# Performance work log

Measured on AMD Instinct MI355X. Metric: run time of the kernel, lower is better.

The kernel has to match this reference:

```python
import jax, jax.numpy as jnp
import numpy as np

S, B, W, D2 = 128, 64, 32, 512   # sen_len, batch, wiki_len, 2*eh_size
DH = 512                          # dh_size


def setup_inputs() -> dict:
    key = jax.random.key(0)
    ks = jax.random.split(key, 8)
    inp = {
        "i": 0,
        "valid_sen": jnp.arange(B, dtype=jnp.int64) if jax.config.jax_enable_x64 else jnp.arange(B, dtype=jnp.int32),
        "reverse_valid_sen": jnp.arange(B, dtype=jnp.int32),
        "wiki_sen": jax.random.randint(ks[0], (B, W, S), 0, 32000),
        "wiki_num": jax.random.randint(ks[1], (B,), 0, W),
        "h1": jax.random.normal(ks[2], (S, B, W, D2), dtype=jnp.float32),
        "h_n1": jax.random.normal(ks[3], (W, B, D2), dtype=jnp.float32),
        "atten_label": jax.random.randint(ks[4], (B,), 0, W),
        "h": jax.random.normal(ks[5], (B, D2), dtype=jnp.float32),
        "h_n": jax.random.normal(ks[6], (B, D2), dtype=jnp.float32),
        # initLinearLayer: Linear(4*eh -> dh)
        "W_init": jax.random.normal(ks[7], (DH, 2 * D2), dtype=jnp.float32) / np.sqrt(2 * D2),
        "b_init": jnp.zeros((DH,), dtype=jnp.float32),
    }
    inp["valid_sen"] = jnp.arange(B, dtype=jnp.int32)
    return inp


def reference(i, valid_sen, reverse_valid_sen, wiki_sen, wiki_num, h1, h_n1,
              atten_label, h, h_n, W_init, b_init):
    # --- gather valid sentences (index_select) ---
    vw_hn1 = h_n1[:, valid_sen]        # [W, Bv, D2]
    v_wiki_sen = wiki_sen[valid_sen]   # [Bv, W, S]
    v_h1 = h1[:, valid_sen]            # [S, Bv, W, D2]
    lbl = atten_label[valid_sen]       # [Bv]

    # --- attention scores: beta[b, w] = <h_n1[w, b], h_n[b]> ---
    beta = jnp.einsum('wbd,bd->bw', vw_hn1, h_n)  # [Bv, W]

    # --- CrossEntropyLoss(ignore_index=0) ---
    logp = jax.nn.log_softmax(beta, axis=1)
    nll = -jnp.take_along_axis(logp, lbl[:, None], axis=1)[:, 0]   # [Bv]
    valid = (lbl != 0)
    cnt = valid.sum().astype(beta.dtype)
    atten_loss = jnp.where(cnt > 0,
                           jnp.sum(jnp.where(valid, nll, 0.0)) / jnp.maximum(cnt, 1.0),
                           0.0)

    # --- golden (scatter one-hot) hard alignment -> context vector ---
    Bv = beta.shape[0]
    b_idx = jnp.arange(Bv)
    wiki_cv = vw_hn1[lbl, b_idx]                   # [Bv, D2]  (== sum over one-hot)

    # --- init hidden for decoder ---
    init_h = jnp.concatenate([h_n, wiki_cv], axis=1) @ W_init.T + b_init  # [Bv, DH]

    # --- select aligned wiki sentence / hidden states ---
    selected_wiki_h = v_h1[:, b_idx, lbl].transpose(1, 0, 2)  # [Bv, S, D2]
    selected_wiki_sen = v_wiki_sen[b_idx, lbl]                # [Bv, S]

    return (selected_wiki_sen, selected_wiki_h, init_h, wiki_cv, atten_loss)
```

## Files before the change

### kernel.cpp

```cpp
#include <hip/hip_runtime.h>

#define S 128
#define B 64
#define W 32
#define D2 512
#define DH 512

typedef float floatx4 __attribute__((ext_vector_type(4)));

#define OFF_SEN 0
#define OFF_SWH (B * S)
#define OFF_INITH (OFF_SWH + B * S * D2)
#define OFF_CV (OFF_INITH + B * DH)
#define OFF_LOSS (OFF_CV + B * D2)


#define NB_BETA 64
#define NB_INITH 128
#define NB_GATHER 512
#define NB_TOTAL (NB_BETA + NB_INITH + NB_GATHER)

__global__ __launch_bounds__(256) void k_fused(
    const float* __restrict__ h1, const float* __restrict__ h_n1,
    const float* __restrict__ h_n, const float* __restrict__ Wi,
    const float* __restrict__ bi, const int* __restrict__ wiki_sen,
    const int* __restrict__ valid_sen, const int* __restrict__ atten_label,
    float* __restrict__ out, float* __restrict__ ws)
{
    __shared__ float smem[4 * 2 * D2];
    const int bid = blockIdx.x;
    const int tid = threadIdx.x;

    if (bid < NB_BETA) {
        const int b = bid;
        const int lane = tid & 63;
        const int wv = tid >> 6;
        const int vs = valid_sen[b];
        const int lbl = atten_label[vs];
        float* sbeta = smem;

        const float* hb = h_n + b * D2;
        const float4 hn0 = ((const float4*)hb)[lane];
        const float4 hn1 = ((const float4*)hb)[64 + lane];

        #pragma unroll
        for (int i = 0; i < 8; ++i) {
            const int w = wv * 8 + i;
            const float* row = h_n1 + (w * B + vs) * D2;
            const float4 a0 = ((const float4*)row)[lane];
            const float4 a1 = ((const float4*)row)[64 + lane];
            float p = a0.x * hn0.x + a0.y * hn0.y + a0.z * hn0.z + a0.w * hn0.w
                    + a1.x * hn1.x + a1.y * hn1.y + a1.z * hn1.z + a1.w * hn1.w;
            #pragma unroll
            for (int m = 32; m >= 1; m >>= 1) p += __shfl_xor(p, m);
            if (lane == 0) sbeta[w] = p;
        }

        if (tid < 128) {
            const float4* src = (const float4*)(h_n1 + (lbl * B + vs) * D2);
            float4* dst = (float4*)(out + OFF_CV + b * D2);
            dst[tid] = src[tid];
        } else {
            const int s = tid - 128;
            out[OFF_SEN + b * S + s] = (float)wiki_sen[(vs * W + lbl) * S + s];
        }
        __syncthreads();

        if (tid == 0) {
            float mx = sbeta[0];
            for (int w = 1; w < W; ++w) mx = fmaxf(mx, sbeta[w]);
            float Z = 0.0f;
            for (int w = 0; w < W; ++w) Z += expf(sbeta[w] - mx);
            const float nll = -(sbeta[lbl] - mx - logf(Z));
            ws[b] = nll;
            ws[B + b] = (lbl != 0) ? 1.0f : 0.0f;
        }
    } else if (bid < NB_BETA + NB_INITH) {
        float (*wrow)[2 * D2] = (float (*)[2 * D2])smem;
        const int kt = (bid - NB_BETA) * 4;

        #pragma unroll
        for (int kk = 0; kk < 4; ++kk) {
            ((float4*)wrow[kk])[tid] =
                ((const float4*)(Wi + (size_t)(kt + kk) * (2 * D2)))[tid];
        }
        __syncthreads();

        const int b = tid >> 2;
        const int kk = tid & 3;
        const int k = kt + kk;
        const int vs = valid_sen[b];
        const int lbl = atten_label[vs];
        float acc = bi[k];
        const float4* hb = (const float4*)(h_n + b * D2);
        const float4* cb = (const float4*)(h_n1 + (lbl * B + vs) * D2);
        const float4* w0 = (const float4*)wrow[kk];
        const float4* w1 = (const float4*)(wrow[kk] + D2);
        #pragma unroll 4
        for (int d = 0; d < D2 / 4; ++d) {
            const float4 a = hb[d], w = w0[d];
            acc += a.x * w.x + a.y * w.y + a.z * w.z + a.w * w.w;
        }
        #pragma unroll 4
        for (int d = 0; d < D2 / 4; ++d) {
            const float4 a = cb[d], w = w1[d];
            acc += a.x * w.x + a.y * w.y + a.z * w.z + a.w * w.w;
        }
        out[OFF_INITH + b * DH + k] = acc;
    } else {
        const int gb = bid - NB_BETA - NB_INITH;
        const int b = gb >> 3;
        const int vs = valid_sen[b];
        const int gi = vs * W + atten_label[vs];

        floatx4 v[8];
        int q[8];
        #pragma unroll
        for (int j = 0; j < 8; ++j) {
            q[j] = gb * 2048 + j * 256 + tid;
            const int t = q[j] >> 7;
            const int s = t & 127;
            const int d4 = q[j] & 127;
            const floatx4* src =
                (const floatx4*)(h1 + ((size_t)(s * (B * W) + gi)) * D2);
            v[j] = __builtin_nontemporal_load(&src[d4]);
        }
        #pragma unroll
        for (int j = 0; j < 8; ++j) {
            __builtin_nontemporal_store(v[j], &((floatx4*)(out + OFF_SWH))[q[j]]);
        }
    }
}

__global__ void k_loss(const float* __restrict__ ws, float* __restrict__ out)
{
    const int t = threadIdx.x;
    float nll = ws[t];
    float v = ws[B + t];
    float sn = v * nll;
    float sc = v;
    #pragma unroll
    for (int m = 32; m >= 1; m >>= 1) {
        sn += __shfl_xor(sn, m);
        sc += __shfl_xor(sc, m);
    }
    if (t == 0) out[OFF_LOSS] = (sc > 0.0f) ? sn / fmaxf(sc, 1.0f) : 0.0f;
}

extern "C" void kernel_launch(void* const* d_in, const int* in_sizes, int n_in,
                              void* d_out, int out_size, void* d_ws, size_t ws_size,
                              hipStream_t stream) {
    const int* valid_sen   = (const int*)d_in[1];
    const int* wiki_sen    = (const int*)d_in[3];
    const float* h1        = (const float*)d_in[5];
    const float* h_n1      = (const float*)d_in[6];
    const int* atten_label = (const int*)d_in[7];
    const float* h_n       = (const float*)d_in[9];
    const float* Wi        = (const float*)d_in[10];
    const float* bi        = (const float*)d_in[11];
    float* out = (float*)d_out;
    float* ws  = (float*)d_ws;

    k_fused<<<NB_TOTAL, 256, 0, stream>>>(h1, h_n1, h_n, Wi, bi, wiki_sen,
                                          valid_sen, atten_label, out, ws);
    k_loss<<<1, 64, 0, stream>>>(ws, out);
}
```

Baseline: 22.00 us.

## Spread the h1 gather across all blocks with a grid-stride split

Every block (beta, init_h, and plain) now takes part in the big selected_wiki_h gather. It uses a grid-stride index with up to 6 float4 loads per thread instead of 8 per thread in dedicated blocks. This balances memory traffic across all 704 blocks so the beta and init_h blocks also contribute bandwidth. In exchange, those blocks carry more work and a longer tail, and each iteration now does per-element index lookups of valid_sen and atten_label.

```diff
diff --git a/kernel.cpp b/kernel.cpp
--- a/kernel.cpp
+++ b/kernel.cpp
@@ -17,8 +17,12 @@
 
 #define NB_BETA 64
 #define NB_INITH 128
-#define NB_GATHER 512
-#define NB_TOTAL (NB_BETA + NB_INITH + NB_GATHER)
+#define NB_PLAIN 512
+#define NB_TOTAL (NB_BETA + NB_INITH + NB_PLAIN)
+
+#define Q_TOTAL (B * S * (D2 / 4))
+#define GSTRIDE (NB_TOTAL * 256)
+#define GCHUNK 6
 
 __global__ __launch_bounds__(256) void k_fused(
     const float* __restrict__ h1, const float* __restrict__ h_n1,
@@ -107,27 +111,32 @@
             acc += a.x * w.x + a.y * w.y + a.z * w.z + a.w * w.w;
         }
         out[OFF_INITH + b * DH + k] = acc;
-    } else {
-        const int gb = bid - NB_BETA - NB_INITH;
-        const int b = gb >> 3;
-        const int vs = valid_sen[b];
-        const int gi = vs * W + atten_label[vs];
+    }
 
-        floatx4 v[8];
-        int q[8];
+    {
+        const int g0 = bid * 256 + tid;
+        floatx4 v[GCHUNK];
+        int q[GCHUNK];
+        bool ok[GCHUNK];
         #pragma unroll
-        for (int j = 0; j < 8; ++j) {
-            q[j] = gb * 2048 + j * 256 + tid;
-            const int t = q[j] >> 7;
-            const int s = t & 127;
-            const int d4 = q[j] & 127;
-            const floatx4* src =
-                (const floatx4*)(h1 + ((size_t)(s * (B * W) + gi)) * D2);
-            v[j] = __builtin_nontemporal_load(&src[d4]);
+        for (int j = 0; j < GCHUNK; ++j) {
+            q[j] = g0 + j * GSTRIDE;
+            ok[j] = (q[j] < Q_TOTAL);
+            if (ok[j]) {
+                const int t = q[j] >> 7;
+                const int s = t & 127;
+                const int b = t >> 7;
+                const int vs = valid_sen[b];
+                const int gi = vs * W + atten_label[vs];
+                const floatx4* src =
+                    (const floatx4*)(h1 + ((size_t)(s * (B * W) + gi)) * D2);
+                v[j] = __builtin_nontemporal_load(&src[q[j] & 127]);
+            }
         }
         #pragma unroll
-        for (int j = 0; j < 8; ++j) {
-            __builtin_nontemporal_store(v[j], &((floatx4*)(out + OFF_SWH))[q[j]]);
+        for (int j = 0; j < GCHUNK; ++j) {
+            if (ok[j])
+                __builtin_nontemporal_store(v[j], &((floatx4*)(out + OFF_SWH))[q[j]]);
         }
     }
 }
```

New measurement: 29.24 us. +32.9%, slower.
